# Kernel tuning notes

Measured on AMD Instinct MI355X. Metric: run time of the kernel, lower is better.

Reference implementation:

```python
import jax, jax.numpy as jnp
import numpy as np

DIM = 2048
NUM_HEADS = 16
HEAD_DIM = DIM // NUM_HEADS
FF_MULT = 2
ROPE_BASE = 10000.0
EPS = 1e-6


def _rmsnorm(x, g):
    return x * jax.lax.rsqrt(jnp.mean(x * x, axis=-1, keepdims=True) + EPS) * g


def _rope_tables(seq_len):
    half = HEAD_DIM // 2
    inv_freq = 1.0 / (ROPE_BASE ** (2.0 * jnp.arange(half, dtype=jnp.float32) / HEAD_DIM))
    angles = jnp.arange(seq_len, dtype=jnp.float32)[:, None] * inv_freq[None, :]  # (S, half)
    return jnp.cos(angles), jnp.sin(angles)


def _apply_rope(x, cos, sin):
    # x: (B, H, S, D); cos/sin: (S, D/2). Interleaved pairs (RoFormer form).
    x_even = x[..., 0::2]
    x_odd = x[..., 1::2]
    c = cos[None, None].astype(x.dtype)
    s = sin[None, None].astype(x.dtype)
    rot_even = x_even * c - x_odd * s
    rot_odd = x_odd * c + x_even * s
    return jnp.stack([rot_even, rot_odd], axis=-1).reshape(x.shape)


def setup_inputs() -> dict:
    key = jax.random.key(0)
    ks = jax.random.split(key, 7)
    B, S = 2, 2048
    scale = 1.0 / np.sqrt(DIM)
    return {
        "x": jax.random.normal(ks[0], (B, S, DIM), dtype=jnp.float32),
        "w_qkv": jax.random.normal(ks[1], (DIM, 3 * DIM), dtype=jnp.float32) * scale,
        "w_out": jax.random.normal(ks[2], (DIM, DIM), dtype=jnp.float32) * scale,
        "w_fc": jax.random.normal(ks[3], (DIM, DIM * FF_MULT), dtype=jnp.float32) * scale,
        "w_proj": jax.random.normal(ks[4], (DIM * FF_MULT, DIM), dtype=jnp.float32) / np.sqrt(DIM * FF_MULT),
        "g_in": jnp.ones((DIM,), dtype=jnp.float32),
        "g_ff": jnp.ones((DIM,), dtype=jnp.float32),
    }


def reference(x, w_qkv, w_out, w_fc, w_proj, g_in, g_ff):
    B, S, D = x.shape
    # --- attention branch ---
    h = _rmsnorm(x, g_in)
    qkv = h @ w_qkv  # (B, S, 3D)
    q, k, v = jnp.split(qkv, 3, axis=-1)
    def heads(t):
        return t.reshape(B, S, NUM_HEADS, HEAD_DIM).transpose(0, 2, 1, 3)
    q, k, v = heads(q), heads(k), heads(v)  # (B, H, S, Dh)
    cos, sin = _rope_tables(S)
    q = _apply_rope(q, cos, sin)
    k = _apply_rope(k, cos, sin)
    scores = jnp.einsum("bhqd,bhkd->bhqk", q, k) / jnp.asarray(np.sqrt(HEAD_DIM), x.dtype)
    causal = jnp.tril(jnp.ones((S, S), dtype=bool))
    scores = jnp.where(causal[None, None], scores, jnp.asarray(-jnp.inf, scores.dtype))
    attn = jax.nn.softmax(scores, axis=-1)
    out = jnp.einsum("bhqk,bhkd->bhqd", attn, v)  # (B, H, S, Dh)
    out = out.transpose(0, 2, 1, 3).reshape(B, S, D)
    x = x + out @ w_out
    # --- feed-forward branch ---
    h = _rmsnorm(x, g_ff)
    x = x + jax.nn.gelu(h @ w_fc) @ w_proj
    return x


if __name__ == "__main__":
    inp = setup_inputs()
    y = reference(**inp)
    print(y.shape, y.dtype)
```

## Files before the change

### kernel.cpp

```cpp
#include <hip/hip_runtime.h>
#include <math.h>

typedef __bf16 bf16x8 __attribute__((ext_vector_type(8)));
typedef float  f32x4  __attribute__((ext_vector_type(4)));

#define DEV __device__ __forceinline__

DEV void gload16(const void* g, void* l) {
  __builtin_amdgcn_global_load_lds(
      (const __attribute__((address_space(1))) void*)g,
      (__attribute__((address_space(3))) void*)l, 16, 0, 0);
}

__global__ __launch_bounds__(256) void transpose_cvt(
    const float* __restrict__ in, __bf16* __restrict__ outT, int R, int C) {
  __shared__ float t[32][33];
  const int c0 = blockIdx.x * 32, r0 = blockIdx.y * 32;
  const int tx = threadIdx.x, ty = threadIdx.y;
#pragma unroll
  for (int i = 0; i < 4; i++)
    t[ty + 8 * i][tx] = in[(size_t)(r0 + ty + 8 * i) * C + c0 + tx];
  __syncthreads();
#pragma unroll
  for (int i = 0; i < 4; i++)
    outT[(size_t)(c0 + ty + 8 * i) * R + r0 + tx] = (__bf16)t[tx][ty + 8 * i];
}

__global__ __launch_bounds__(256) void rmsnorm_kernel(
    const float* __restrict__ x, const float* __restrict__ g, __bf16* __restrict__ out) {
  const int r = blockIdx.x, t = threadIdx.x;
  const float4* xr = (const float4*)(x + (size_t)r * 2048);
  float4 a = xr[2 * t], b = xr[2 * t + 1];
  float ss = a.x * a.x + a.y * a.y + a.z * a.z + a.w * a.w +
             b.x * b.x + b.y * b.y + b.z * b.z + b.w * b.w;
#pragma unroll
  for (int mk = 1; mk < 64; mk <<= 1) ss += __shfl_xor(ss, mk);
  __shared__ float red[4];
  if ((t & 63) == 0) red[t >> 6] = ss;
  __syncthreads();
  const float sc = rsqrtf((red[0] + red[1] + red[2] + red[3]) * (1.0f / 2048.0f) + 1e-6f);
  const float4* gr = (const float4*)g;
  float4 ga = gr[2 * t], gb = gr[2 * t + 1];
  bf16x8 ov;
  ov[0] = (__bf16)(a.x * sc * ga.x); ov[1] = (__bf16)(a.y * sc * ga.y);
  ov[2] = (__bf16)(a.z * sc * ga.z); ov[3] = (__bf16)(a.w * sc * ga.w);
  ov[4] = (__bf16)(b.x * sc * gb.x); ov[5] = (__bf16)(b.y * sc * gb.y);
  ov[6] = (__bf16)(b.z * sc * gb.z); ov[7] = (__bf16)(b.w * sc * gb.w);
  *(bf16x8*)(out + (size_t)r * 2048 + t * 8) = ov;
}

template <int EPI>
__global__ __launch_bounds__(256) void gemm_bt(
    const __bf16* __restrict__ A, const __bf16* __restrict__ BT,
    void* __restrict__ Cout, const float* __restrict__ res, int M, int N, int K) {
  __shared__ char lds[32768];
  char* As = lds;
  char* Bs = lds + 16384;
  const int tid = threadIdx.x;
  const int lane = tid & 63;
  const int bn = blockIdx.x, bm = blockIdx.y;
  const int wm = tid >> 7, wn = (tid >> 6) & 1;

  f32x4 acc[4][4];
#pragma unroll
  for (int i = 0; i < 4; i++)
#pragma unroll
    for (int j = 0; j < 4; j++) acc[i][j] = (f32x4){0.f, 0.f, 0.f, 0.f};

  const size_t strideA = (size_t)K * 2;
  const char* ga[4];
  const char* gb[4];
#pragma unroll
  for (int t = 0; t < 4; t++) {
    int gg = t * 256 + tid;
    int row = gg >> 3, slot = gg & 7;
    ga[t] = (const char*)A + (size_t)(bm * 128 + row) * strideA + ((slot ^ (row & 7)) << 4);
    gb[t] = (const char*)BT + (size_t)(bn * 128 + row) * strideA + ((slot ^ (row & 7)) << 4);
  }

  for (int k0 = 0; k0 < K; k0 += 64) {
    __syncthreads();
#pragma unroll
    for (int t = 0; t < 4; t++) {
      int gg = t * 256 + tid;
      gload16(ga[t], As + gg * 16);
      gload16(gb[t], Bs + gg * 16);
      ga[t] += 128;
      gb[t] += 128;
    }
    __syncthreads();
#pragma unroll
    for (int kk = 0; kk < 2; kk++) {
      bf16x8 a[4], b[4];
      const int c16 = kk * 4 + (lane >> 4);
#pragma unroll
      for (int i = 0; i < 4; i++) {
        int ra = wm * 64 + i * 16 + (lane & 15);
        a[i] = *(const bf16x8*)(As + ra * 128 + ((c16 ^ (ra & 7)) << 4));
        int rb = wn * 64 + i * 16 + (lane & 15);
        b[i] = *(const bf16x8*)(Bs + rb * 128 + ((c16 ^ (rb & 7)) << 4));
      }
#pragma unroll
      for (int i = 0; i < 4; i++)
#pragma unroll
        for (int j = 0; j < 4; j++)
          acc[i][j] = __builtin_amdgcn_mfma_f32_16x16x32_bf16(a[i], b[j], acc[i][j], 0, 0, 0);
    }
  }

#pragma unroll
  for (int i = 0; i < 4; i++)
#pragma unroll
    for (int j = 0; j < 4; j++)
#pragma unroll
      for (int r = 0; r < 4; r++) {
        int row = bm * 128 + wm * 64 + i * 16 + ((lane >> 4) << 2) + r;
        int col = bn * 128 + wn * 64 + j * 16 + (lane & 15);
        size_t idx = (size_t)row * N + col;
        float v = acc[i][j][r];
        if (EPI == 0) {
          ((__bf16*)Cout)[idx] = (__bf16)v;
        } else if (EPI == 1) {
          ((float*)Cout)[idx] = v + res[idx];
        } else {
          float u = 0.7978845608028654f * (v + 0.044715f * v * v * v);
          ((__bf16*)Cout)[idx] = (__bf16)(0.5f * v * (1.0f + tanhf(u)));
        }
      }
}

__global__ __launch_bounds__(256) void rope_tables(float* __restrict__ tab) {
  const int idx = blockIdx.x * 256 + threadIdx.x;
  const int s = idx >> 6, j = idx & 63;
  const float inv = powf(10000.0f, -(float)j / 64.0f);
  const float a = (float)s * inv;
  tab[idx] = cosf(a);
  tab[131072 + idx] = sinf(a);
}

__global__ __launch_bounds__(256) void rope_apply(
    const __bf16* __restrict__ qkv, const float* __restrict__ tab,
    __bf16* __restrict__ qr, __bf16* __restrict__ kr) {
  const int idx = blockIdx.x * 256 + threadIdx.x;
  const int j = idx & 63;
  const int h = (idx >> 6) & 15;
  const int s = (idx >> 10) & 2047;
  const int b = idx >> 21;
  const float c = tab[(s << 6) + j], sn = tab[131072 + (s << 6) + j];
  const size_t qi = ((size_t)(b * 2048 + s)) * 6144 + h * 128 + 2 * j;
  const size_t qo = ((size_t)((b * 16 + h) * 2048 + s)) * 128 + 2 * j;
  {
    float e = (float)qkv[qi], o = (float)qkv[qi + 1];
    qr[qo] = (__bf16)(e * c - o * sn);
    qr[qo + 1] = (__bf16)(o * c + e * sn);
  }
  {
    float e = (float)qkv[qi + 2048], o = (float)qkv[qi + 2048 + 1];
    kr[qo] = (__bf16)(e * c - o * sn);
    kr[qo + 1] = (__bf16)(o * c + e * sn);
  }
}

__global__ __launch_bounds__(256) void v_transpose(
    const __bf16* __restrict__ qkv, __bf16* __restrict__ vt) {
  __shared__ __bf16 t[32][33];
  const int s0 = blockIdx.x * 32, d0 = blockIdx.y * 32, bh = blockIdx.z;
  const int b = bh >> 4, h = bh & 15;
  const int tx = threadIdx.x, ty = threadIdx.y;
#pragma unroll
  for (int i = 0; i < 4; i++)
    t[ty + 8 * i][tx] =
        qkv[((size_t)(b * 2048 + s0 + ty + 8 * i)) * 6144 + 4096 + h * 128 + d0 + tx];
  __syncthreads();
#pragma unroll
  for (int i = 0; i < 4; i++)
    vt[((size_t)bh * 128 + d0 + ty + 8 * i) * 2048 + s0 + tx] = t[tx][ty + 8 * i];
}

__global__ __launch_bounds__(256) void flash_attn(
    const __bf16* __restrict__ qg, const __bf16* __restrict__ kg,
    const __bf16* __restrict__ vtg, __bf16* __restrict__ og) {
  __shared__ char lds[73728];
  const int tid = threadIdx.x, lane = tid & 63, w = tid >> 6;
  const int h = blockIdx.y, b = blockIdx.z;
  const int bh = b * 16 + h;
  const __bf16* qb = qg + (size_t)bh * 2048 * 128;
  const char* kbb = (const char*)(kg + (size_t)bh * 2048 * 128);
  const char* vbb = (const char*)(vtg + (size_t)bh * 128 * 2048);
  char* Pw = lds + 65536 + w * 2048;

  const char* gK[4];
  const char* gV[4];
#pragma unroll
  for (int t = 0; t < 4; t++) {
    int gg = t * 256 + tid;
    int rk = gg >> 4, sk = gg & 15;
    gK[t] = kbb + rk * 256 + ((sk ^ (rk & 15)) << 4);
    int rv = gg >> 3, sv = gg & 7;
    gV[t] = vbb + rv * 4096 + ((sv ^ (rv & 7)) << 4);
  }

  const float SL2E = 0.08838834764831845f * 1.4426950408889634f;

  auto run_qtile = [&](int qt) {
    const int qrow0 = qt * 64 + w * 16;
    bf16x8 qf[4];
#pragma unroll
    for (int c = 0; c < 4; c++) {
      bf16x8 raw = *(const bf16x8*)(qb + (size_t)(qrow0 + (lane & 15)) * 128 +
                                    c * 32 + ((lane >> 4) << 3));
#pragma unroll
      for (int e = 0; e < 8; e++) qf[c][e] = (__bf16)((float)raw[e] * SL2E);
    }
    float m[4], ls[4];
    f32x4 o[8];
#pragma unroll
    for (int r = 0; r < 4; r++) { m[r] = -__builtin_inff(); ls[r] = 0.f; }
#pragma unroll
    for (int n = 0; n < 8; n++) o[n] = (f32x4){0.f, 0.f, 0.f, 0.f};

#pragma unroll
    for (int t = 0; t < 4; t++) {
      int gg = t * 256 + tid;
      gload16(gK[t], lds + gg * 16);
      gload16(gV[t], lds + 32768 + gg * 16);
    }

    for (int kt = 0; kt <= qt; kt++) {
      const int cur = kt & 1;
      char* Ks = lds + cur * 16384;
      char* Vs = lds + 32768 + cur * 16384;
      if (kt < qt) {
        char* Kd = lds + (cur ^ 1) * 16384;
        char* Vd = lds + 32768 + (cur ^ 1) * 16384;
#pragma unroll
        for (int t = 0; t < 4; t++) {
          int gg = t * 256 + tid;
          gload16(gK[t] + (size_t)(kt + 1) * 16384, Kd + gg * 16);
          gload16(gV[t] + (size_t)(kt + 1) * 128, Vd + gg * 16);
        }
        asm volatile("s_waitcnt vmcnt(8)" ::: "memory");
      } else {
        asm volatile("s_waitcnt vmcnt(0)" ::: "memory");
      }
      __builtin_amdgcn_s_barrier();

      f32x4 s[4];
      __builtin_amdgcn_s_setprio(1);
#pragma unroll
      for (int n = 0; n < 4; n++) {
        s[n] = (f32x4){0.f, 0.f, 0.f, 0.f};
#pragma unroll
        for (int c = 0; c < 4; c++) {
          int krow = n * 16 + (lane & 15);
          int c16 = c * 4 + (lane >> 4);
          bf16x8 kf = *(const bf16x8*)(Ks + krow * 256 + ((c16 ^ (krow & 15)) << 4));
          s[n] = __builtin_amdgcn_mfma_f32_16x16x32_bf16(qf[c], kf, s[n], 0, 0, 0);
        }
      }
      __builtin_amdgcn_s_setprio(0);

      float p[4][4], fc[4];
      const bool diag = (kt == qt);
#pragma unroll
      for (int r = 0; r < 4; r++) {
        if (diag) {
          const int qrow = qrow0 + ((lane >> 4) << 2) + r;
#pragma unroll
          for (int n = 0; n < 4; n++) {
            int col = kt * 64 + n * 16 + (lane & 15);
            if (col > qrow) s[n][r] = -__builtin_inff();
          }
        }
        float tmx = fmaxf(fmaxf(s[0][r], s[1][r]), fmaxf(s[2][r], s[3][r]));
#pragma unroll
        for (int mk = 1; mk < 16; mk <<= 1) tmx = fmaxf(tmx, __shfl_xor(tmx, mk));
        float nm;
        if (tmx <= m[r] + 8.f) {
          nm = m[r];
          fc[r] = 1.f;
        } else {
          nm = tmx;
          fc[r] = exp2f(m[r] - nm);
          m[r] = nm;
        }
        float sum = 0.f;
#pragma unroll
        for (int n = 0; n < 4; n++) {
          float pv = exp2f(s[n][r] - nm);
          p[n][r] = pv;
          sum += pv;
        }
#pragma unroll
        for (int mk = 1; mk < 16; mk <<= 1) sum += __shfl_xor(sum, mk);
        ls[r] = ls[r] * fc[r] + sum;
      }
      if ((fc[0] < 1.f) | (fc[1] < 1.f) | (fc[2] < 1.f) | (fc[3] < 1.f)) {
#pragma unroll
        for (int n = 0; n < 8; n++) {
          o[n][0] *= fc[0]; o[n][1] *= fc[1]; o[n][2] *= fc[2]; o[n][3] *= fc[3];
        }
      }

#pragma unroll
      for (int n = 0; n < 4; n++)
#pragma unroll
        for (int r = 0; r < 4; r++) {
          int prow = ((lane >> 4) << 2) + r;
          int col = n * 16 + (lane & 15);
          int ch = col >> 3;
          *(__bf16*)(Pw + prow * 128 + ((ch ^ (prow & 7)) << 4) + ((col & 7) << 1)) =
              (__bf16)p[n][r];
        }

      __builtin_amdgcn_s_setprio(1);
#pragma unroll
      for (int kk = 0; kk < 2; kk++) {
        int prow = lane & 15;
        int pc = kk * 4 + (lane >> 4);
        bf16x8 pf = *(const bf16x8*)(Pw + prow * 128 + ((pc ^ (prow & 7)) << 4));
#pragma unroll
        for (int n = 0; n < 8; n++) {
          int vr = n * 16 + (lane & 15);
          bf16x8 vf = *(const bf16x8*)(Vs + vr * 128 + ((pc ^ (vr & 7)) << 4));
          o[n] = __builtin_amdgcn_mfma_f32_16x16x32_bf16(pf, vf, o[n], 0, 0, 0);
        }
      }
      __builtin_amdgcn_s_setprio(0);
      __builtin_amdgcn_s_barrier();
    }

    float inv[4];
#pragma unroll
    for (int r = 0; r < 4; r++) inv[r] = 1.0f / ls[r];
#pragma unroll
    for (int n = 0; n < 8; n++)
#pragma unroll
      for (int r = 0; r < 4; r++) {
        int qrow = qrow0 + ((lane >> 4) << 2) + r;
        og[(size_t)(b * 2048 + qrow) * 2048 + h * 128 + n * 16 + (lane & 15)] =
            (__bf16)(o[n][r] * inv[r]);
      }
  };

  run_qtile(31 - (int)blockIdx.x);
  run_qtile((int)blockIdx.x);
}

extern "C" void kernel_launch(void* const* d_in, const int* in_sizes, int n_in,
                              void* d_out, int out_size, void* d_ws, size_t ws_size,
                              hipStream_t stream) {
  const float* x = (const float*)d_in[0];
  const float* w_qkv = (const float*)d_in[1];
  const float* w_out = (const float*)d_in[2];
  const float* w_fc = (const float*)d_in[3];
  const float* w_proj = (const float*)d_in[4];
  const float* g_in = (const float*)d_in[5];
  const float* g_ff = (const float*)d_in[6];
  float* out = (float*)d_out;
  char* ws = (char*)d_ws;

  constexpr size_t O_WQKV = 0;
  constexpr size_t O_WOUT = 25165824;
  constexpr size_t O_WFC = 33554432;
  constexpr size_t O_WPROJ = 50331648;
  constexpr size_t O_H = 67108864;
  constexpr size_t O_QKV = 83886080;
  constexpr size_t O_Q = 134217728;
  constexpr size_t O_K = 150994944;
  constexpr size_t O_VT = 167772160;
  constexpr size_t O_TAB = 184549376;
  constexpr size_t O_ATTN = 185597952;
  constexpr size_t O_X1 = 202375168;

  __bf16* wqkvT = (__bf16*)(ws + O_WQKV);
  __bf16* woutT = (__bf16*)(ws + O_WOUT);
  __bf16* wfcT = (__bf16*)(ws + O_WFC);
  __bf16* wprojT = (__bf16*)(ws + O_WPROJ);
  __bf16* h = (__bf16*)(ws + O_H);
  __bf16* qkv = (__bf16*)(ws + O_QKV);
  __bf16* fcact = (__bf16*)(ws + O_QKV);
  __bf16* qr = (__bf16*)(ws + O_Q);
  __bf16* kr = (__bf16*)(ws + O_K);
  __bf16* vt = (__bf16*)(ws + O_VT);
  float* tab = (float*)(ws + O_TAB);
  __bf16* attn = (__bf16*)(ws + O_ATTN);
  float* x1 = (float*)(ws + O_X1);

  const dim3 tb(32, 8);
  transpose_cvt<<<dim3(6144 / 32, 2048 / 32), tb, 0, stream>>>(w_qkv, wqkvT, 2048, 6144);
  transpose_cvt<<<dim3(2048 / 32, 2048 / 32), tb, 0, stream>>>(w_out, woutT, 2048, 2048);
  transpose_cvt<<<dim3(4096 / 32, 2048 / 32), tb, 0, stream>>>(w_fc, wfcT, 2048, 4096);
  transpose_cvt<<<dim3(2048 / 32, 4096 / 32), tb, 0, stream>>>(w_proj, wprojT, 4096, 2048);

  rmsnorm_kernel<<<4096, 256, 0, stream>>>(x, g_in, h);
  gemm_bt<0><<<dim3(48, 32), 256, 0, stream>>>(h, wqkvT, (void*)qkv, nullptr, 4096, 6144, 2048);
  rope_tables<<<512, 256, 0, stream>>>(tab);
  rope_apply<<<16384, 256, 0, stream>>>(qkv, tab, qr, kr);
  v_transpose<<<dim3(64, 4, 32), tb, 0, stream>>>(qkv, vt);
  flash_attn<<<dim3(16, 16, 2), 256, 0, stream>>>(qr, kr, vt, attn);
  gemm_bt<1><<<dim3(16, 32), 256, 0, stream>>>(attn, woutT, (void*)x1, x, 4096, 2048, 2048);
  rmsnorm_kernel<<<4096, 256, 0, stream>>>(x1, g_ff, h);
  gemm_bt<2><<<dim3(32, 32), 256, 0, stream>>>(h, wfcT, (void*)fcact, nullptr, 4096, 4096, 2048);
  gemm_bt<1><<<dim3(16, 32), 256, 0, stream>>>(fcact, wprojT, (void*)out, x1, 4096, 2048, 4096);
}
```

Baseline: 551.6 us.

## Add 256x256-tile 8-wave GEMM with phased MFMA scheduling for QKV and FC

New measurement: 560.1 us. About the same (+1.5%).

```diff
diff --git a/kernel.cpp b/kernel.cpp
--- a/kernel.cpp
+++ b/kernel.cpp
@@ -116,6 +116,154 @@
       for (int r = 0; r < 4; r++) {
         int row = bm * 128 + wm * 64 + i * 16 + ((lane >> 4) << 2) + r;
         int col = bn * 128 + wn * 64 + j * 16 + (lane & 15);
+        size_t idx = (size_t)row * N + col;
+        float v = acc[i][j][r];
+        if (EPI == 0) {
+          ((__bf16*)Cout)[idx] = (__bf16)v;
+        } else if (EPI == 1) {
+          ((float*)Cout)[idx] = v + res[idx];
+        } else {
+          float u = 0.7978845608028654f * (v + 0.044715f * v * v * v);
+          ((__bf16*)Cout)[idx] = (__bf16)(0.5f * v * (1.0f + tanhf(u)));
+        }
+      }
+}
+
+template <int EPI>
+__global__ __launch_bounds__(512, 2) void gemm256(
+    const __bf16* __restrict__ A, const __bf16* __restrict__ BT,
+    void* __restrict__ Cout, const float* __restrict__ res, int M, int N, int K) {
+  __shared__ char lds[131072];
+  const int tid = threadIdx.x;
+  const int lane = tid & 63;
+  const int w = tid >> 6;
+  const int wm = w >> 2;
+  const int wn = w & 3;
+  const int bn = blockIdx.x, bm = blockIdx.y;
+
+  f32x4 acc[8][4];
+#pragma unroll
+  for (int i = 0; i < 8; i++)
+#pragma unroll
+    for (int j = 0; j < 4; j++) acc[i][j] = (f32x4){0.f, 0.f, 0.f, 0.f};
+
+  const size_t strideA = (size_t)K * 2;
+  const char* gA[4];
+  const char* gB[4];
+#pragma unroll
+  for (int t = 0; t < 4; t++) {
+    int gg = t * 512 + tid;
+    int row = gg >> 3, slot = gg & 7;
+    gA[t] = (const char*)A + (size_t)(bm * 256 + row) * strideA + ((slot ^ (row & 7)) << 4);
+    gB[t] = (const char*)BT + (size_t)(bn * 256 + row) * strideA + ((slot ^ (row & 7)) << 4);
+  }
+
+  auto stage8 = [&](int kt, int buf) {
+    const size_t koff = (size_t)kt * 128;
+    char* Ad = lds + buf * 32768;
+    char* Bd = lds + 65536 + buf * 32768;
+#pragma unroll
+    for (int t = 0; t < 4; t++) {
+      gload16(gA[t] + koff, Ad + (t * 512 + tid) * 16);
+      gload16(gB[t] + koff, Bd + (t * 512 + tid) * 16);
+    }
+  };
+
+  const int NT = K >> 6;
+  stage8(0, 0);
+
+  for (int kt = 0; kt < NT; ++kt) {
+    const int buf = kt & 1;
+    const char* Ab = lds + buf * 32768;
+    const char* Bb = lds + 65536 + buf * 32768;
+    const int ktp = (kt + 1 < NT) ? kt + 1 : kt;
+    stage8(ktp, buf ^ 1);
+    asm volatile("s_waitcnt vmcnt(8)" ::: "memory");
+    __builtin_amdgcn_s_barrier();
+
+    bf16x8 a[4][2], b0[2][2], b1[2][2];
+#pragma unroll
+    for (int i = 0; i < 4; i++)
+#pragma unroll
+      for (int kk = 0; kk < 2; kk++) {
+        int ra = wm * 128 + i * 16 + (lane & 15);
+        int c16 = kk * 4 + (lane >> 4);
+        a[i][kk] = *(const bf16x8*)(Ab + ra * 128 + ((c16 ^ (ra & 7)) << 4));
+      }
+#pragma unroll
+    for (int j = 0; j < 2; j++)
+#pragma unroll
+      for (int kk = 0; kk < 2; kk++) {
+        int rb = wn * 64 + j * 16 + (lane & 15);
+        int c16 = kk * 4 + (lane >> 4);
+        b0[j][kk] = *(const bf16x8*)(Bb + rb * 128 + ((c16 ^ (rb & 7)) << 4));
+      }
+    __builtin_amdgcn_s_setprio(1);
+#pragma unroll
+    for (int i = 0; i < 4; i++)
+#pragma unroll
+      for (int j = 0; j < 2; j++)
+#pragma unroll
+        for (int kk = 0; kk < 2; kk++)
+          acc[i][j] = __builtin_amdgcn_mfma_f32_16x16x32_bf16(a[i][kk], b0[j][kk], acc[i][j], 0, 0, 0);
+    __builtin_amdgcn_s_setprio(0);
+#pragma unroll
+    for (int j = 0; j < 2; j++)
+#pragma unroll
+      for (int kk = 0; kk < 2; kk++) {
+        int rb = wn * 64 + (2 + j) * 16 + (lane & 15);
+        int c16 = kk * 4 + (lane >> 4);
+        b1[j][kk] = *(const bf16x8*)(Bb + rb * 128 + ((c16 ^ (rb & 7)) << 4));
+      }
+    __builtin_amdgcn_s_barrier();
+    __builtin_amdgcn_s_setprio(1);
+#pragma unroll
+    for (int i = 0; i < 4; i++)
+#pragma unroll
+      for (int j = 0; j < 2; j++)
+#pragma unroll
+        for (int kk = 0; kk < 2; kk++)
+          acc[i][2 + j] = __builtin_amdgcn_mfma_f32_16x16x32_bf16(a[i][kk], b1[j][kk], acc[i][2 + j], 0, 0, 0);
+    __builtin_amdgcn_s_setprio(0);
+#pragma unroll
+    for (int i = 0; i < 4; i++)
+#pragma unroll
+      for (int kk = 0; kk < 2; kk++) {
+        int ra = wm * 128 + 64 + i * 16 + (lane & 15);
+        int c16 = kk * 4 + (lane >> 4);
+        a[i][kk] = *(const bf16x8*)(Ab + ra * 128 + ((c16 ^ (ra & 7)) << 4));
+      }
+    __builtin_amdgcn_s_barrier();
+    __builtin_amdgcn_s_setprio(1);
+#pragma unroll
+    for (int i = 0; i < 4; i++)
+#pragma unroll
+      for (int j = 0; j < 2; j++)
+#pragma unroll
+        for (int kk = 0; kk < 2; kk++)
+          acc[4 + i][2 + j] = __builtin_amdgcn_mfma_f32_16x16x32_bf16(a[i][kk], b1[j][kk], acc[4 + i][2 + j], 0, 0, 0);
+    __builtin_amdgcn_s_setprio(0);
+    __builtin_amdgcn_s_barrier();
+    __builtin_amdgcn_s_setprio(1);
+#pragma unroll
+    for (int i = 0; i < 4; i++)
+#pragma unroll
+      for (int j = 0; j < 2; j++)
+#pragma unroll
+        for (int kk = 0; kk < 2; kk++)
+          acc[4 + i][j] = __builtin_amdgcn_mfma_f32_16x16x32_bf16(a[i][kk], b0[j][kk], acc[4 + i][j], 0, 0, 0);
+    __builtin_amdgcn_s_setprio(0);
+    __builtin_amdgcn_s_barrier();
+  }
+
+#pragma unroll
+  for (int i = 0; i < 8; i++)
+#pragma unroll
+    for (int j = 0; j < 4; j++)
+#pragma unroll
+      for (int r = 0; r < 4; r++) {
+        int row = bm * 256 + wm * 128 + i * 16 + ((lane >> 4) << 2) + r;
+        int col = bn * 256 + wn * 64 + j * 16 + (lane & 15);
         size_t idx = (size_t)row * N + col;
         float v = acc[i][j][r];
         if (EPI == 0) {
@@ -394,13 +542,13 @@
   transpose_cvt<<<dim3(2048 / 32, 4096 / 32), tb, 0, stream>>>(w_proj, wprojT, 4096, 2048);
 
   rmsnorm_kernel<<<4096, 256, 0, stream>>>(x, g_in, h);
-  gemm_bt<0><<<dim3(48, 32), 256, 0, stream>>>(h, wqkvT, (void*)qkv, nullptr, 4096, 6144, 2048);
+  gemm256<0><<<dim3(24, 16), 512, 0, stream>>>(h, wqkvT, (void*)qkv, nullptr, 4096, 6144, 2048);
   rope_tables<<<512, 256, 0, stream>>>(tab);
   rope_apply<<<16384, 256, 0, stream>>>(qkv, tab, qr, kr);
   v_transpose<<<dim3(64, 4, 32), tb, 0, stream>>>(qkv, vt);
   flash_attn<<<dim3(16, 16, 2), 256, 0, stream>>>(qr, kr, vt, attn);
   gemm_bt<1><<<dim3(16, 32), 256, 0, stream>>>(attn, woutT, (void*)x1, x, 4096, 2048, 2048);
   rmsnorm_kernel<<<4096, 256, 0, stream>>>(x1, g_ff, h);
-  gemm_bt<2><<<dim3(32, 32), 256, 0, stream>>>(h, wfcT, (void*)fcact, nullptr, 4096, 4096, 2048);
+  gemm256<2><<<dim3(16, 16), 512, 0, stream>>>(h, wfcT, (void*)fcact, nullptr, 4096, 4096, 2048);
   gemm_bt<1><<<dim3(16, 32), 256, 0, stream>>>(fcact, wprojT, (void*)out, x1, 4096, 2048, 4096);
 }
```

## Use 128-row query tiles with 8 waves and lazy softmax rescaling in flash attention

Applied to the files above, without the earlier changes.

Result: faster. 520.9 us (-5.6%).

```diff
diff --git a/kernel.cpp b/kernel.cpp
--- a/kernel.cpp
+++ b/kernel.cpp
@@ -177,10 +177,10 @@
     vt[((size_t)bh * 128 + d0 + ty + 8 * i) * 2048 + s0 + tx] = t[tx][ty + 8 * i];
 }
 
-__global__ __launch_bounds__(256) void flash_attn(
+__global__ __launch_bounds__(512) void flash_attn(
     const __bf16* __restrict__ qg, const __bf16* __restrict__ kg,
     const __bf16* __restrict__ vtg, __bf16* __restrict__ og) {
-  __shared__ char lds[73728];
+  __shared__ char lds[81920];
   const int tid = threadIdx.x, lane = tid & 63, w = tid >> 6;
   const int h = blockIdx.y, b = blockIdx.z;
   const int bh = b * 16 + h;
@@ -189,11 +189,11 @@
   const char* vbb = (const char*)(vtg + (size_t)bh * 128 * 2048);
   char* Pw = lds + 65536 + w * 2048;
 
-  const char* gK[4];
-  const char* gV[4];
-#pragma unroll
-  for (int t = 0; t < 4; t++) {
-    int gg = t * 256 + tid;
+  const char* gK[2];
+  const char* gV[2];
+#pragma unroll
+  for (int t = 0; t < 2; t++) {
+    int gg = t * 512 + tid;
     int rk = gg >> 4, sk = gg & 15;
     gK[t] = kbb + rk * 256 + ((sk ^ (rk & 15)) << 4);
     int rv = gg >> 3, sv = gg & 7;
@@ -202,8 +202,17 @@
 
   const float SL2E = 0.08838834764831845f * 1.4426950408889634f;
 
+  auto stageKV = [&](int kt, int buf) {
+#pragma unroll
+    for (int t = 0; t < 2; t++) {
+      int gg = t * 512 + tid;
+      gload16(gK[t] + (size_t)kt * 16384, lds + buf * 16384 + gg * 16);
+      gload16(gV[t] + (size_t)kt * 128, lds + 32768 + buf * 16384 + gg * 16);
+    }
+  };
+
   auto run_qtile = [&](int qt) {
-    const int qrow0 = qt * 64 + w * 16;
+    const int qrow0 = qt * 128 + w * 16;
     bf16x8 qf[4];
 #pragma unroll
     for (int c = 0; c < 4; c++) {
@@ -212,34 +221,23 @@
 #pragma unroll
       for (int e = 0; e < 8; e++) qf[c][e] = (__bf16)((float)raw[e] * SL2E);
     }
-    float m[4], ls[4];
+    float m[4], lsp[4];
     f32x4 o[8];
 #pragma unroll
-    for (int r = 0; r < 4; r++) { m[r] = -__builtin_inff(); ls[r] = 0.f; }
+    for (int r = 0; r < 4; r++) { m[r] = -__builtin_inff(); lsp[r] = 0.f; }
 #pragma unroll
     for (int n = 0; n < 8; n++) o[n] = (f32x4){0.f, 0.f, 0.f, 0.f};
 
-#pragma unroll
-    for (int t = 0; t < 4; t++) {
-      int gg = t * 256 + tid;
-      gload16(gK[t], lds + gg * 16);
-      gload16(gV[t], lds + 32768 + gg * 16);
-    }
-
-    for (int kt = 0; kt <= qt; kt++) {
+    const int NKT = 2 * qt + 2;
+    stageKV(0, 0);
+
+    for (int kt = 0; kt < NKT; kt++) {
       const int cur = kt & 1;
-      char* Ks = lds + cur * 16384;
-      char* Vs = lds + 32768 + cur * 16384;
-      if (kt < qt) {
-        char* Kd = lds + (cur ^ 1) * 16384;
-        char* Vd = lds + 32768 + (cur ^ 1) * 16384;
-#pragma unroll
-        for (int t = 0; t < 4; t++) {
-          int gg = t * 256 + tid;
-          gload16(gK[t] + (size_t)(kt + 1) * 16384, Kd + gg * 16);
-          gload16(gV[t] + (size_t)(kt + 1) * 128, Vd + gg * 16);
-        }
-        asm volatile("s_waitcnt vmcnt(8)" ::: "memory");
+      const char* Ks = lds + cur * 16384;
+      const char* Vs = lds + 32768 + cur * 16384;
+      if (kt < NKT - 1) {
+        stageKV(kt + 1, cur ^ 1);
+        asm volatile("s_waitcnt vmcnt(4)" ::: "memory");
       } else {
         asm volatile("s_waitcnt vmcnt(0)" ::: "memory");
       }
@@ -260,11 +258,9 @@
       }
       __builtin_amdgcn_s_setprio(0);
 
-      float p[4][4], fc[4];
-      const bool diag = (kt == qt);
-#pragma unroll
-      for (int r = 0; r < 4; r++) {
-        if (diag) {
+      if (kt * 64 + 63 > qrow0) {
+#pragma unroll
+        for (int r = 0; r < 4; r++) {
           const int qrow = qrow0 + ((lane >> 4) << 2) + r;
 #pragma unroll
           for (int n = 0; n < 4; n++) {
@@ -272,34 +268,43 @@
             if (col > qrow) s[n][r] = -__builtin_inff();
           }
         }
-        float tmx = fmaxf(fmaxf(s[0][r], s[1][r]), fmaxf(s[2][r], s[3][r]));
-#pragma unroll
-        for (int mk = 1; mk < 16; mk <<= 1) tmx = fmaxf(tmx, __shfl_xor(tmx, mk));
-        float nm;
-        if (tmx <= m[r] + 8.f) {
-          nm = m[r];
-          fc[r] = 1.f;
-        } else {
-          nm = tmx;
-          fc[r] = exp2f(m[r] - nm);
+      }
+
+      float tmx[4];
+#pragma unroll
+      for (int r = 0; r < 4; r++)
+        tmx[r] = fmaxf(fmaxf(s[0][r], s[1][r]), fmaxf(s[2][r], s[3][r]));
+      bool hot = (tmx[0] > m[0] + 8.f) | (tmx[1] > m[1] + 8.f) |
+                 (tmx[2] > m[2] + 8.f) | (tmx[3] > m[3] + 8.f);
+      if (__any(hot)) {
+        float fc[4];
+#pragma unroll
+        for (int r = 0; r < 4; r++) {
+          float gmx = tmx[r];
+#pragma unroll
+          for (int mk = 1; mk < 16; mk <<= 1) gmx = fmaxf(gmx, __shfl_xor(gmx, mk));
+          float nm = fmaxf(m[r], gmx);
+          fc[r] = __builtin_amdgcn_exp2f(m[r] - nm);
           m[r] = nm;
-        }
+          lsp[r] *= fc[r];
+        }
+#pragma unroll
+        for (int n = 0; n < 8; n++) {
+          o[n][0] *= fc[0]; o[n][1] *= fc[1]; o[n][2] *= fc[2]; o[n][3] *= fc[3];
+        }
+      }
+
+      float p[4][4];
+#pragma unroll
+      for (int r = 0; r < 4; r++) {
         float sum = 0.f;
 #pragma unroll
         for (int n = 0; n < 4; n++) {
-          float pv = exp2f(s[n][r] - nm);
+          float pv = __builtin_amdgcn_exp2f(s[n][r] - m[r]);
           p[n][r] = pv;
           sum += pv;
         }
-#pragma unroll
-        for (int mk = 1; mk < 16; mk <<= 1) sum += __shfl_xor(sum, mk);
-        ls[r] = ls[r] * fc[r] + sum;
-      }
-      if ((fc[0] < 1.f) | (fc[1] < 1.f) | (fc[2] < 1.f) | (fc[3] < 1.f)) {
-#pragma unroll
-        for (int n = 0; n < 8; n++) {
-          o[n][0] *= fc[0]; o[n][1] *= fc[1]; o[n][2] *= fc[2]; o[n][3] *= fc[3];
-        }
+        lsp[r] += sum;
       }
 
 #pragma unroll
@@ -332,7 +337,12 @@
 
     float inv[4];
 #pragma unroll
-    for (int r = 0; r < 4; r++) inv[r] = 1.0f / ls[r];
+    for (int r = 0; r < 4; r++) {
+      float ls = lsp[r];
+#pragma unroll
+      for (int mk = 1; mk < 16; mk <<= 1) ls += __shfl_xor(ls, mk);
+      inv[r] = 1.0f / ls;
+    }
 #pragma unroll
     for (int n = 0; n < 8; n++)
 #pragma unroll
@@ -343,7 +353,7 @@
       }
   };
 
-  run_qtile(31 - (int)blockIdx.x);
+  run_qtile(15 - (int)blockIdx.x);
   run_qtile((int)blockIdx.x);
 }
 
@@ -398,7 +408,7 @@
   rope_tables<<<512, 256, 0, stream>>>(tab);
   rope_apply<<<16384, 256, 0, stream>>>(qkv, tab, qr, kr);
   v_transpose<<<dim3(64, 4, 32), tb, 0, stream>>>(qkv, vt);
-  flash_attn<<<dim3(16, 16, 2), 256, 0, stream>>>(qr, kr, vt, attn);
+  flash_attn<<<dim3(8, 16, 2), 512, 0, stream>>>(qr, kr, vt, attn);
   gemm_bt<1><<<dim3(16, 32), 256, 0, stream>>>(attn, woutT, (void*)x1, x, 4096, 2048, 2048);
   rmsnorm_kernel<<<4096, 256, 0, stream>>>(x1, g_ff, h);
   gemm_bt<2><<<dim3(32, 32), 256, 0, stream>>>(h, wfcT, (void*)fcact, nullptr, 4096, 4096, 2048);
```
